# Performance work log

Measured on AMD Instinct MI355X. Metric: run time of the kernel, lower is better.

Reference implementation:

```python
import jax, jax.numpy as jnp
import numpy as np

L = 104          # atom feature / hidden dim (self.length)
NUM_CLASSES = 500
D, N, P = 256, 1024, 8  # DAGs, nodes per DAG (topo-ordered), max predecessors


def setup_inputs() -> dict:
    key = jax.random.key(0)
    ks = jax.random.split(key, 8)
    atom_features = jax.random.normal(ks[0], (D, N, L), dtype=jnp.float32)

    # Padded predecessor lists; pred_idx[d, n, p] < n guarantees topological order 0..N-1.
    rng = np.random.default_rng(0)
    base = np.floor(rng.random((D, N, P)) * np.maximum(np.arange(N), 1)[None, :, None]).astype(np.int32)
    keep = rng.random((D, N, P)) < 0.6
    keep[:, :, 0] = True                      # every non-root node has >=1 predecessor
    pred_idx = np.where(keep, base, -1)
    pred_idx[:, 0, :] = -1                    # node 0 is the root (no predecessors)
    pred_idx = jnp.asarray(pred_idx, dtype=jnp.int32)

    s1 = float(1.0 / np.sqrt(L))
    s2 = float(1.0 / np.sqrt(2 * L))
    W_single = jax.random.uniform(ks[1], (L, L), minval=-s1, maxval=s1)
    b_single = jax.random.uniform(ks[2], (L,), minval=-s1, maxval=s1)
    W_merge = jax.random.uniform(ks[3], (L, 2 * L), minval=-s2, maxval=s2)
    b_merge = jax.random.uniform(ks[4], (L,), minval=-s2, maxval=s2)
    attn_w = jax.random.uniform(ks[5], (L,))   # torch.rand(length)
    dag_w = jax.random.uniform(ks[6], (L,))
    W_final = jax.random.uniform(ks[7], (NUM_CLASSES, L), minval=-s1, maxval=s1)
    b_final = jnp.zeros((NUM_CLASSES,), jnp.float32)
    return {
        "atom_features": atom_features, "pred_idx": pred_idx,
        "W_single": W_single, "b_single": b_single,
        "W_merge": W_merge, "b_merge": b_merge,
        "attn_w": attn_w, "dag_w": dag_w,
        "W_final": W_final, "b_final": b_final,
    }


def _forward(atom_features, pred_idx, W_single, b_single, W_merge, b_merge,
             attn_w, dag_w, W_final, b_final):
    n_nodes = atom_features.shape[1]

    def per_dag(feats, preds):  # feats [N, L], preds [N, P]
        def step(outputs, n):
            feat = feats[n]                                   # [L]
            p = preds[n]                                      # [P]
            valid = p >= 0                                    # [P]
            po = outputs[jnp.clip(p, 0, n_nodes - 1)]         # [P, L] gathered predecessor outputs
            # softmax over the predecessor (stacking) dim, weighted by attention_weight
            logits = jnp.where(valid[:, None], attn_w * po, -1e30)
            agg = jnp.sum(jax.nn.softmax(logits, axis=0) * po * valid[:, None].astype(po.dtype), axis=0)  # [L]
            merged = jax.nn.relu(W_merge @ jnp.concatenate([agg, feat]) + b_merge)
            root = jax.nn.relu(W_single @ feat + b_single)
            out = jnp.where(jnp.any(valid), merged, root)     # [L]
            return outputs.at[n].set(out), None
        outputs, _ = jax.lax.scan(step, jnp.zeros_like(feats), jnp.arange(n_nodes))
        return outputs[-1]                                    # output of last (sink) node

    last = jax.vmap(per_dag)(atom_features, pred_idx)         # [D, L]
    w = jax.nn.softmax(dag_w * last, axis=0)                  # softmax over DAG dim
    pooled = jnp.sum(w * last, axis=0)                        # [L]
    return pooled @ W_final.T + b_final                       # [NUM_CLASSES]


def reference(atom_features, pred_idx, W_single, b_single, W_merge, b_merge,
              attn_w, dag_w, W_final, b_final):
    return _forward(atom_features, pred_idx, W_single, b_single, W_merge, b_merge,
                    attn_w, dag_w, W_final, b_final)
```

## Files before the change

kernel.cpp:

```cpp
#include <hip/hip_runtime.h>

#define DN  256
#define NN  1024
#define PP  8
#define LL  104
#define CLS 500
#define BT  512
#define TMAX 64
#define KP  232
#define NG  26
#define OLP 108
#define NEGBIG -3.0e38f

typedef __attribute__((ext_vector_type(8))) short short8;
typedef __attribute__((ext_vector_type(4))) short short4v;
typedef __attribute__((ext_vector_type(4))) float f32x4;

#define MFMA(a, b, c) __builtin_amdgcn_mfma_f32_16x16x32_bf16((a), (b), (c), 0, 0, 0)

#define BAR_RAW() do {                                              \
    __builtin_amdgcn_sched_barrier(0);                              \
    asm volatile("s_waitcnt lgkmcnt(0)" ::: "memory");              \
    __builtin_amdgcn_s_barrier();                                   \
    __builtin_amdgcn_sched_barrier(0);                              \
} while (0)

__device__ __forceinline__ void split_bf16(float x, unsigned short& h, unsigned short& l) {
    unsigned u = __float_as_uint(x);
    h = (unsigned short)(u >> 16);
    float hf = __uint_as_float(u & 0xFFFF0000u);
    l = (unsigned short)(__float_as_uint(x - hf) >> 16);
}

__device__ __forceinline__ void sm_store3(int ni, int lg, float4 aw4,
    const float4 pv[PP], float4 ft,
    unsigned short (*xh)[KP], unsigned short (*xl)[KP])
{
    float awv[4] = {aw4.x, aw4.y, aw4.z, aw4.w};
    float ftv[4] = {ft.x, ft.y, ft.z, ft.w};
    unsigned short oh[4], ol[4], fh[4], fl[4];
    #pragma unroll
    for (int f = 0; f < 4; ++f) {
        float den = 0.f, num = 0.f;
        #pragma unroll
        for (int q = 0; q < PP; ++q) {
            float pvq = ((const float*)&pv[q])[f];
            float e2 = exp2f(awv[f] * pvq);
            den += e2;
            num = fmaf(e2, pvq, num);
        }
        float agg = __fdividef(num, den);
        split_bf16(agg,    oh[f], ol[f]);
        split_bf16(ftv[f], fh[f], fl[f]);
    }
    *(short4v*)&xh[ni][lg*4] = (short4v){(short)oh[0],(short)oh[1],(short)oh[2],(short)oh[3]};
    *(short4v*)&xl[ni][lg*4] = (short4v){(short)ol[0],(short)ol[1],(short)ol[2],(short)ol[3]};
    *(short4v*)&xh[ni][LL + lg*4] = (short4v){(short)fh[0],(short)fh[1],(short)fh[2],(short)fh[3]};
    *(short4v*)&xl[ni][LL + lg*4] = (short4v){(short)fl[0],(short)fl[1],(short)fl[2],(short)fl[3]};
}

__global__ __launch_bounds__(BT, 2) void dag_level_kernel(
    const float* __restrict__ atom,
    const int*   __restrict__ pred,
    const float* __restrict__ W_single,
    const float* __restrict__ b_single,
    const float* __restrict__ W_merge,
    const float* __restrict__ b_merge,
    const float* __restrict__ attn_w,
    float* __restrict__ out_all,
    float* __restrict__ last_buf)
{
    __shared__ __align__(16) unsigned short x_hi[TMAX][KP];
    __shared__ __align__(16) unsigned short x_lo[TMAX][KP];
    __shared__ __align__(16) unsigned short ppos_lds[NN][PP];
    __shared__ __align__(16) float out_lds[2][TMAX][OLP];
    __shared__ int   lvl[NN];
    __shared__ int   cnt[NN];
    __shared__ unsigned short order[NN];
    __shared__ unsigned short pos_lds[NN];
    __shared__ __align__(16) float s_attn2[LL];
    __shared__ float s_bm[LL];
    __shared__ int   csum[64];
    __shared__ int   s_flag, s_maxlvl;

    const int d    = blockIdx.x;
    const int tid  = threadIdx.x;
    const int wid  = tid >> 6;
    const int lane = tid & 63;
    const int my_ni = tid / NG;
    const int my_lg = tid - my_ni * NG;

    const float* atom_d = atom + (size_t)d * NN * LL;
    const int*   pred_d = pred + (size_t)d * NN * PP;
    float*       out_d  = out_all + (size_t)d * NN * LL;

    short8 wh[7], wl[7];
    {
        const int r = min(wid, 6)*16 + (lane & 15);
        #pragma unroll
        for (int kt = 0; kt < 7; ++kt) {
            const int k0 = kt*32 + (lane >> 4)*8;
            short8 hh, lo8;
            #pragma unroll
            for (int j = 0; j < 8; ++j) {
                float v = (r < LL && (k0 + j) < 2*LL) ? W_merge[r*2*LL + k0 + j] : 0.f;
                unsigned short a, b;
                split_bf16(v, a, b);
                hh[j] = (short)a; lo8[j] = (short)b;
            }
            wh[kt] = hh; wl[kt] = lo8;
        }
    }

    for (int idx = tid; idx < TMAX * (KP - 2*LL); idx += BT) {
        int rr = idx / (KP - 2*LL), cc = 2*LL + (idx - rr*(KP - 2*LL));
        x_hi[rr][cc] = 0; x_lo[rr][cc] = 0;
    }
    if (tid < LL) {
        s_attn2[tid] = fmaxf(attn_w[tid] * 1.44269504f, 1e-30f);
        s_bm[tid] = b_merge[tid];
    }
    if (tid == 0) { s_flag = 0; s_maxlvl = 0; }
    lvl[tid] = 0; lvl[tid + BT] = 0;

    int mypA[PP], mypB[PP];
    {
        const int4* p4 = (const int4*)(pred_d + tid * PP);
        int4 a = p4[0], b = p4[1];
        mypA[0]=a.x; mypA[1]=a.y; mypA[2]=a.z; mypA[3]=a.w;
        mypA[4]=b.x; mypA[5]=b.y; mypA[6]=b.z; mypA[7]=b.w;
        const int4* q4 = (const int4*)(pred_d + (tid + BT) * PP);
        int4 c = q4[0], e = q4[1];
        mypB[0]=c.x; mypB[1]=c.y; mypB[2]=c.z; mypB[3]=c.w;
        mypB[4]=e.x; mypB[5]=e.y; mypB[6]=e.z; mypB[7]=e.w;
    }
    __syncthreads();

    for (int it = 1; it <= NN; ++it) {
        bool ch = false;
        #pragma unroll
        for (int rep = 0; rep < 2; ++rep) {
            int mxA = -1, mxB = -1;
            #pragma unroll
            for (int q = 0; q < PP; ++q) {
                if (mypA[q] >= 0) mxA = max(mxA, lvl[mypA[q]]);
                if (mypB[q] >= 0) mxB = max(mxB, lvl[mypB[q]]);
            }
            if (mxA + 1 != lvl[tid])      { lvl[tid]      = mxA + 1; ch = true; }
            if (mxB + 1 != lvl[tid + BT]) { lvl[tid + BT] = mxB + 1; ch = true; }
        }
        if (ch) s_flag = it;
        __syncthreads();
        int f = s_flag;
        __syncthreads();
        if (f != it) break;
    }
    atomicMax(&s_maxlvl, max(lvl[tid], lvl[tid + BT]));

    cnt[tid] = 0; cnt[tid + BT] = 0;
    __syncthreads();
    atomicAdd(&cnt[lvl[tid]], 1);
    atomicAdd(&cnt[lvl[tid + BT]], 1);
    __syncthreads();
    if (tid < 64) { int s = 0; for (int i = 0; i < 16; ++i) s += cnt[tid*16 + i]; csum[tid] = s; }
    __syncthreads();
    if (tid == 0) { int run = 0; for (int t = 0; t < 64; ++t) { int c = csum[t]; csum[t] = run; run += c; } }
    __syncthreads();
    if (tid < 64) {
        int run = csum[tid];
        for (int i = 0; i < 16; ++i) { int c = cnt[tid*16 + i]; cnt[tid*16 + i] = run; run += c; }
    }
    __syncthreads();
    {
        int pos = atomicAdd(&cnt[lvl[tid]], 1);
        order[pos] = (unsigned short)tid;        pos_lds[tid] = (unsigned short)pos;
        pos = atomicAdd(&cnt[lvl[tid + BT]], 1);
        order[pos] = (unsigned short)(tid + BT); pos_lds[tid + BT] = (unsigned short)pos;
    }
    __syncthreads();

    {
        unsigned short tA[PP], tB[PP];
        #pragma unroll
        for (int q = 0; q < PP; ++q) {
            tA[q] = (mypA[q] < 0) ? (unsigned short)0xFFFFu : pos_lds[mypA[q]];
            tB[q] = (mypB[q] < 0) ? (unsigned short)0xFFFFu : pos_lds[mypB[q]];
        }
        int pA = pos_lds[tid], pB = pos_lds[tid + BT];
        *(short4v*)&ppos_lds[pA][0] = (short4v){(short)tA[0],(short)tA[1],(short)tA[2],(short)tA[3]};
        *(short4v*)&ppos_lds[pA][4] = (short4v){(short)tA[4],(short)tA[5],(short)tA[6],(short)tA[7]};
        *(short4v*)&ppos_lds[pB][0] = (short4v){(short)tB[0],(short)tB[1],(short)tB[2],(short)tB[3]};
        *(short4v*)&ppos_lds[pB][4] = (short4v){(short)tB[4],(short)tB[5],(short)tB[6],(short)tB[7]};
    }
    __syncthreads();

    const float4 my_aw = *(const float4*)&s_attn2[my_lg * 4];

    {
        int nroots = cnt[0];
        for (int task = tid; task < nroots * LL; task += BT) {
            int ni = task / LL, r = task - ni * LL;
            int n = order[ni];
            float acc = b_single[r];
            const float* feat = atom_d + n * LL;
            const float* wr = W_single + r * LL;
            #pragma unroll 8
            for (int l = 0; l < LL; ++l) acc = fmaf(wr[l], feat[l], acc);
            float v = fmaxf(acc, 0.f);
            out_d[n * LL + r] = v;
            if (ni < TMAX) out_lds[1][ni][r] = v;
            if (n == NN - 1) last_buf[d * LL + r] = v;
        }
    }
    __syncthreads();

    const int maxlvl = s_maxlvl;

    float4  pf_po[PP];
    float4  pf_ft = {0.f,0.f,0.f,0.f};
    short8  pf_pps = {0,0,0,0,0,0,0,0};

#define PREFETCH(NT0, NTC, CT0, PT0, PBUF) do {                                \
        if (tid < (NTC) * NG) {                                                \
            int n_ = order[(NT0) + my_ni];                                     \
            pf_ft  = *(const float4*)&atom_d[n_ * LL + my_lg * 4];             \
            pf_pps = *(const short8*)&ppos_lds[(NT0) + my_ni][0];              \
            _Pragma("unroll")                                                  \
            for (int q_ = 0; q_ < PP; ++q_) {                                  \
                int pp_ = (unsigned short)pf_pps[q_];                          \
                if (pp_ >= (CT0)) {                                            \
                    pf_po[q_] = (float4){NEGBIG, NEGBIG, NEGBIG, NEGBIG};      \
                } else if (pp_ >= (PT0)) {                                     \
                    pf_po[q_] = *(const float4*)&out_lds[PBUF][pp_ - (PT0)][my_lg * 4]; \
                } else {                                                       \
                    pf_po[q_] = *(const float4*)&out_d[(int)order[pp_] * LL + my_lg * 4]; \
                }                                                              \
            }                                                                  \
        }                                                                      \
    } while (0)

    int pt0 = 0, ptc = cnt[0];
    int wbuf = 0;

    if (maxlvl >= 1) {
        int s1 = cnt[0];
        PREFETCH(s1, min(TMAX, cnt[1] - s1), s1, 0, 1);
    }

    for (int L = 1; L <= maxlvl; ++L) {
        const int s = cnt[L - 1], e = cnt[L];
        for (int t0 = s; t0 < e; t0 += TMAX) {
            const int tc = min(TMAX, e - t0);
            const int ntask = tc * NG;
            const int pcopy = ptc * NG;
            const int rbuf = wbuf ^ 1;

            for (int ct = tid; ct < pcopy; ct += BT) {
                int ci = ct / NG, lg2 = ct - ci * NG;
                *(float4*)&out_d[(int)order[pt0 + ci] * LL + lg2 * 4] =
                    *(const float4*)&out_lds[rbuf][ci][lg2 * 4];
            }
            if (tid < ntask) {
                float4 pv[PP];
                #pragma unroll
                for (int q = 0; q < PP; ++q) {
                    int pp = (unsigned short)pf_pps[q];
                    bool fresh = (pp >= pt0) && (pp < t0);
                    int slot = fresh ? (pp - pt0) : 0;
                    float4 lv = *(const float4*)&out_lds[rbuf][slot][my_lg * 4];
                    pv[q] = fresh ? lv : pf_po[q];
                }
                sm_store3(my_ni, my_lg, my_aw, pv, pf_ft, x_hi, x_lo);
            }
            for (int task = tid + BT; task < ntask; task += BT) {
                int ni = task / NG, lg = task - ni * NG;
                short8 pps = *(const short8*)&ppos_lds[t0 + ni][0];
                float4 pv[PP];
                #pragma unroll
                for (int q = 0; q < PP; ++q) {
                    int pp = (unsigned short)pps[q];
                    if (pp >= t0) {
                        pv[q] = (float4){NEGBIG, NEGBIG, NEGBIG, NEGBIG};
                    } else if (pp >= pt0) {
                        pv[q] = *(const float4*)&out_lds[rbuf][pp - pt0][lg * 4];
                    } else {
                        pv[q] = *(const float4*)&out_d[(int)order[pp] * LL + lg * 4];
                    }
                }
                int n = order[t0 + ni];
                float4 ft = *(const float4*)&atom_d[n * LL + lg * 4];
                float4 aw4 = *(const float4*)&s_attn2[lg * 4];
                sm_store3(ni, lg, aw4, pv, ft, x_hi, x_lo);
            }
            __syncthreads();

            {
                int nt0 = 0, ntc = 0;
                if (t0 + TMAX < e)        { nt0 = t0 + TMAX; ntc = min(TMAX, e - nt0); }
                else if (L + 1 <= maxlvl) { nt0 = e;         ntc = min(TMAX, cnt[L + 1] - e); }
                PREFETCH(nt0, ntc, t0, pt0, rbuf);
            }

            if (wid < 7) {
                const int mts = (tc + 15) >> 4;
                const int kg = (lane >> 4) * 8;
                const int r0 = wid*16 + (lane & 15);
                for (int mt = 0; mt < mts; ++mt) {
                    const int row_a = mt*16 + (lane & 15);
                    f32x4 a0 = {0.f,0.f,0.f,0.f}, b0 = {0.f,0.f,0.f,0.f}, c0 = {0.f,0.f,0.f,0.f};
                    #pragma unroll
                    for (int kt = 0; kt < 7; ++kt) {
                        const int k0 = kt*32 + kg;
                        short8 ah = *(const short8*)&x_hi[row_a][k0];
                        short8 al = *(const short8*)&x_lo[row_a][k0];
                        a0 = MFMA(ah, wh[kt], a0);
                        b0 = MFMA(ah, wl[kt], b0);
                        c0 = MFMA(al, wh[kt], c0);
                    }
                    f32x4 acc = a0 + b0 + c0;
                    if (r0 < LL) {
                        #pragma unroll
                        for (int j = 0; j < 4; ++j) {
                            int ni = mt*16 + (lane >> 4)*4 + j;
                            if (ni < tc) {
                                float v = fmaxf(acc[j] + s_bm[r0], 0.f);
                                out_lds[wbuf][ni][r0] = v;
                                int n = order[t0 + ni];
                                if (n == NN - 1) last_buf[d*LL + r0] = v;
                            }
                        }
                    }
                }
            }
            BAR_RAW();
            pt0 = t0; ptc = tc; wbuf ^= 1;
        }
    }
#undef PREFETCH
}

__global__ __launch_bounds__(256) void final_pool_kernel(
    const float* __restrict__ last_buf,
    const float* __restrict__ dag_w,
    const float* __restrict__ W_final,
    const float* __restrict__ b_final,
    float* __restrict__ out)
{
    __shared__ float s_pooled[LL];
    const int tid = threadIdx.x;

    if (tid < LL) {
        float dw = dag_w[tid];
        float m = -1e30f;
        #pragma unroll 8
        for (int dd = 0; dd < DN; ++dd)
            m = fmaxf(m, dw * last_buf[dd * LL + tid]);
        float den = 0.f, num = 0.f;
        #pragma unroll 8
        for (int dd = 0; dd < DN; ++dd) {
            float v = last_buf[dd * LL + tid];
            float e = __expf(dw * v - m);
            den += e;
            num = fmaf(e, v, num);
        }
        s_pooled[tid] = num / den;
    }
    __syncthreads();

    for (int c = tid; c < CLS; c += 256) {
        float acc = b_final[c];
        const float* wr = W_final + c * LL;
        #pragma unroll 8
        for (int l = 0; l < LL; ++l) acc = fmaf(wr[l], s_pooled[l], acc);
        out[c] = acc;
    }
}

extern "C" void kernel_launch(void* const* d_in, const int* in_sizes, int n_in,
                              void* d_out, int out_size, void* d_ws, size_t ws_size,
                              hipStream_t stream) {
    const float* atom     = (const float*)d_in[0];
    const int*   pred     = (const int*)  d_in[1];
    const float* W_single = (const float*)d_in[2];
    const float* b_single = (const float*)d_in[3];
    const float* W_merge  = (const float*)d_in[4];
    const float* b_merge  = (const float*)d_in[5];
    const float* attn_w   = (const float*)d_in[6];
    const float* dag_w    = (const float*)d_in[7];
    const float* W_final  = (const float*)d_in[8];
    const float* b_final  = (const float*)d_in[9];
    float* out = (float*)d_out;

    float* out_all  = (float*)d_ws;
    float* last_buf = out_all + (size_t)DN * NN * LL;

    dag_level_kernel<<<DN, BT, 0, stream>>>(atom, pred, W_single, b_single,
                                            W_merge, b_merge, attn_w,
                                            out_all, last_buf);
    final_pool_kernel<<<1, 256, 0, stream>>>(last_buf, dag_w, W_final, b_final, out);
}
```

Measured before the change: 378.8 us.

## Accumulate prefetched softmax partials incrementally instead of holding raw predecessor vectors

The prefetch stage now folds the exp2 numerator and denominator of already-available predecessors into running float4 partial sums, and pre-splits features into bf16 hi/lo halves. It no longer keeps eight raw float4 predecessor rows in registers. The global-memory loads are issued before the MFMA section and consumed after it, so their latency is hidden behind the matrix work. The intent is to cut register pressure and shorten the serial aggregation after the barrier. In exchange, the code is more complex and masks invalid entries with NEGBIG exponent inputs instead of using branches.

Measured after the change: 400.9 us. 5.8% more time.

```diff
diff --git a/kernel.cpp b/kernel.cpp
--- a/kernel.cpp
+++ b/kernel.cpp
@@ -32,31 +32,37 @@
     l = (unsigned short)(__float_as_uint(x - hf) >> 16);
 }
 
-__device__ __forceinline__ void sm_store3(int ni, int lg, float4 aw4,
-    const float4 pv[PP], float4 ft,
-    unsigned short (*xh)[KP], unsigned short (*xl)[KP])
+__device__ __forceinline__ void split4(float4 v, short4v& h4, short4v& l4) {
+    unsigned short h0,h1,h2,h3,l0,l1,l2,l3;
+    split_bf16(v.x,h0,l0); split_bf16(v.y,h1,l1);
+    split_bf16(v.z,h2,l2); split_bf16(v.w,h3,l3);
+    h4 = (short4v){(short)h0,(short)h1,(short)h2,(short)h3};
+    l4 = (short4v){(short)l0,(short)l1,(short)l2,(short)l3};
+}
+
+__device__ __forceinline__ void acc4(float4& num, float4& den, float4 aw, float4 v, bool on) {
+    float e0 = __builtin_amdgcn_exp2f(on ? aw.x*v.x : NEGBIG);
+    float e1 = __builtin_amdgcn_exp2f(on ? aw.y*v.y : NEGBIG);
+    float e2 = __builtin_amdgcn_exp2f(on ? aw.z*v.z : NEGBIG);
+    float e3 = __builtin_amdgcn_exp2f(on ? aw.w*v.w : NEGBIG);
+    den.x += e0; den.y += e1; den.z += e2; den.w += e3;
+    num.x = fmaf(e0, v.x, num.x);
+    num.y = fmaf(e1, v.y, num.y);
+    num.z = fmaf(e2, v.z, num.z);
+    num.w = fmaf(e3, v.w, num.w);
+}
+
+__device__ __forceinline__ void store_x(int ni, int lg, float4 num, float4 den,
+    short4v fth, short4v ftl, unsigned short (*xh)[KP], unsigned short (*xl)[KP])
 {
-    float awv[4] = {aw4.x, aw4.y, aw4.z, aw4.w};
-    float ftv[4] = {ft.x, ft.y, ft.z, ft.w};
-    unsigned short oh[4], ol[4], fh[4], fl[4];
-    #pragma unroll
-    for (int f = 0; f < 4; ++f) {
-        float den = 0.f, num = 0.f;
-        #pragma unroll
-        for (int q = 0; q < PP; ++q) {
-            float pvq = ((const float*)&pv[q])[f];
-            float e2 = exp2f(awv[f] * pvq);
-            den += e2;
-            num = fmaf(e2, pvq, num);
-        }
-        float agg = __fdividef(num, den);
-        split_bf16(agg,    oh[f], ol[f]);
-        split_bf16(ftv[f], fh[f], fl[f]);
-    }
-    *(short4v*)&xh[ni][lg*4] = (short4v){(short)oh[0],(short)oh[1],(short)oh[2],(short)oh[3]};
-    *(short4v*)&xl[ni][lg*4] = (short4v){(short)ol[0],(short)ol[1],(short)ol[2],(short)ol[3]};
-    *(short4v*)&xh[ni][LL + lg*4] = (short4v){(short)fh[0],(short)fh[1],(short)fh[2],(short)fh[3]};
-    *(short4v*)&xl[ni][LL + lg*4] = (short4v){(short)fl[0],(short)fl[1],(short)fl[2],(short)fl[3]};
+    float4 agg = { __fdividef(num.x, den.x), __fdividef(num.y, den.y),
+                   __fdividef(num.z, den.z), __fdividef(num.w, den.w) };
+    short4v ah, al;
+    split4(agg, ah, al);
+    *(short4v*)&xh[ni][lg*4] = ah;
+    *(short4v*)&xl[ni][lg*4] = al;
+    *(short4v*)&xh[ni][LL + lg*4] = fth;
+    *(short4v*)&xl[ni][LL + lg*4] = ftl;
 }
 
 __global__ __launch_bounds__(BT, 2) void dag_level_kernel(
@@ -216,35 +222,22 @@
 
     const int maxlvl = s_maxlvl;
 
-    float4  pf_po[PP];
-    float4  pf_ft = {0.f,0.f,0.f,0.f};
+    float4  pf_num = {0,0,0,0}, pf_den = {0,0,0,0};
+    short4v pf_fth = {0,0,0,0}, pf_ftl = {0,0,0,0};
     short8  pf_pps = {0,0,0,0,0,0,0,0};
-
-#define PREFETCH(NT0, NTC, CT0, PT0, PBUF) do {                                \
-        if (tid < (NTC) * NG) {                                                \
-            int n_ = order[(NT0) + my_ni];                                     \
-            pf_ft  = *(const float4*)&atom_d[n_ * LL + my_lg * 4];             \
-            pf_pps = *(const short8*)&ppos_lds[(NT0) + my_ni][0];              \
-            _Pragma("unroll")                                                  \
-            for (int q_ = 0; q_ < PP; ++q_) {                                  \
-                int pp_ = (unsigned short)pf_pps[q_];                          \
-                if (pp_ >= (CT0)) {                                            \
-                    pf_po[q_] = (float4){NEGBIG, NEGBIG, NEGBIG, NEGBIG};      \
-                } else if (pp_ >= (PT0)) {                                     \
-                    pf_po[q_] = *(const float4*)&out_lds[PBUF][pp_ - (PT0)][my_lg * 4]; \
-                } else {                                                       \
-                    pf_po[q_] = *(const float4*)&out_d[(int)order[pp_] * LL + my_lg * 4]; \
-                }                                                              \
-            }                                                                  \
-        }                                                                      \
-    } while (0)
 
     int pt0 = 0, ptc = cnt[0];
     int wbuf = 0;
 
     if (maxlvl >= 1) {
         int s1 = cnt[0];
-        PREFETCH(s1, min(TMAX, cnt[1] - s1), s1, 0, 1);
+        int ntc0 = min(TMAX, cnt[1] - s1);
+        if (tid < ntc0 * NG) {
+            int n_ = order[s1 + my_ni];
+            float4 ft = *(const float4*)&atom_d[n_ * LL + my_lg * 4];
+            split4(ft, pf_fth, pf_ftl);
+            pf_pps = *(const short8*)&ppos_lds[s1 + my_ni][0];
+        }
     }
 
     for (int L = 1; L <= maxlvl; ++L) {
@@ -261,44 +254,79 @@
                     *(const float4*)&out_lds[rbuf][ci][lg2 * 4];
             }
             if (tid < ntask) {
-                float4 pv[PP];
+                float4 num = pf_num, den = pf_den;
                 #pragma unroll
                 for (int q = 0; q < PP; ++q) {
                     int pp = (unsigned short)pf_pps[q];
                     bool fresh = (pp >= pt0) && (pp < t0);
                     int slot = fresh ? (pp - pt0) : 0;
                     float4 lv = *(const float4*)&out_lds[rbuf][slot][my_lg * 4];
-                    pv[q] = fresh ? lv : pf_po[q];
-                }
-                sm_store3(my_ni, my_lg, my_aw, pv, pf_ft, x_hi, x_lo);
+                    acc4(num, den, my_aw, lv, fresh);
+                }
+                store_x(my_ni, my_lg, num, den, pf_fth, pf_ftl, x_hi, x_lo);
             }
             for (int task = tid + BT; task < ntask; task += BT) {
                 int ni = task / NG, lg = task - ni * NG;
                 short8 pps = *(const short8*)&ppos_lds[t0 + ni][0];
-                float4 pv[PP];
+                float4 aw4 = *(const float4*)&s_attn2[lg * 4];
+                float4 gv2[PP];
                 #pragma unroll
                 for (int q = 0; q < PP; ++q) {
                     int pp = (unsigned short)pps[q];
-                    if (pp >= t0) {
-                        pv[q] = (float4){NEGBIG, NEGBIG, NEGBIG, NEGBIG};
-                    } else if (pp >= pt0) {
-                        pv[q] = *(const float4*)&out_lds[rbuf][pp - pt0][lg * 4];
-                    } else {
-                        pv[q] = *(const float4*)&out_d[(int)order[pp] * LL + lg * 4];
-                    }
+                    bool old = pp < pt0;
+                    int row = old ? (int)order[pp] : 0;
+                    gv2[q] = *(const float4*)&out_d[row * LL + lg * 4];
+                }
+                float4 num = {0,0,0,0}, den = {0,0,0,0};
+                #pragma unroll
+                for (int q = 0; q < PP; ++q) {
+                    int pp = (unsigned short)pps[q];
+                    bool on   = pp < t0;
+                    bool prev = pp >= pt0;
+                    int slot = (prev && on) ? (pp - pt0) : 0;
+                    float4 lv = *(const float4*)&out_lds[rbuf][slot][lg * 4];
+                    float4 v;
+                    v.x = prev ? lv.x : gv2[q].x; v.y = prev ? lv.y : gv2[q].y;
+                    v.z = prev ? lv.z : gv2[q].z; v.w = prev ? lv.w : gv2[q].w;
+                    acc4(num, den, aw4, v, on);
                 }
                 int n = order[t0 + ni];
                 float4 ft = *(const float4*)&atom_d[n * LL + lg * 4];
-                float4 aw4 = *(const float4*)&s_attn2[lg * 4];
-                sm_store3(ni, lg, aw4, pv, ft, x_hi, x_lo);
+                short4v fth, ftl;
+                split4(ft, fth, ftl);
+                store_x(ni, lg, num, den, fth, ftl, x_hi, x_lo);
             }
             __syncthreads();
 
-            {
-                int nt0 = 0, ntc = 0;
-                if (t0 + TMAX < e)        { nt0 = t0 + TMAX; ntc = min(TMAX, e - nt0); }
-                else if (L + 1 <= maxlvl) { nt0 = e;         ntc = min(TMAX, cnt[L + 1] - e); }
-                PREFETCH(nt0, ntc, t0, pt0, rbuf);
+            int nt0 = 0, ntc = 0;
+            if (t0 + TMAX < e)        { nt0 = t0 + TMAX; ntc = min(TMAX, e - nt0); }
+            else if (L + 1 <= maxlvl) { nt0 = e;         ntc = min(TMAX, cnt[L + 1] - e); }
+            const bool pf_act = tid < ntc * NG;
+
+            float4 gv[PP];
+            float4 ft4 = {0.f, 0.f, 0.f, 0.f};
+            if (pf_act) {
+                int n_ = order[nt0 + my_ni];
+                ft4 = *(const float4*)&atom_d[n_ * LL + my_lg * 4];
+                pf_pps = *(const short8*)&ppos_lds[nt0 + my_ni][0];
+                #pragma unroll
+                for (int q = 0; q < PP; ++q) {
+                    int pp = (unsigned short)pf_pps[q];
+                    bool old = pp < pt0;
+                    int row = old ? (int)order[pp] : 0;
+                    gv[q] = *(const float4*)&out_d[row * LL + my_lg * 4];
+                }
+            }
+            pf_num = (float4){0,0,0,0}; pf_den = (float4){0,0,0,0};
+            if (pf_act) {
+                #pragma unroll
+                for (int q = 0; q < PP; ++q) {
+                    int pp = (unsigned short)pf_pps[q];
+                    bool prev = (pp >= pt0) && (pp < t0);
+                    int slot = prev ? (pp - pt0) : 0;
+                    float4 lv = *(const float4*)&out_lds[rbuf][slot][my_lg * 4];
+                    acc4(pf_num, pf_den, my_aw, lv, prev);
+                }
             }
 
             if (wid < 7) {
@@ -332,11 +360,21 @@
                     }
                 }
             }
+
+            if (pf_act) {
+                #pragma unroll
+                for (int q = 0; q < PP; ++q) {
+                    int pp = (unsigned short)pf_pps[q];
+                    bool old = pp < pt0;
+                    acc4(pf_num, pf_den, my_aw, gv[q], old);
+                }
+                split4(ft4, pf_fth, pf_ftl);
+            }
+
             BAR_RAW();
             pt0 = t0; ptc = tc; wbuf ^= 1;
         }
     }
-#undef PREFETCH
 }
 
 __global__ __launch_bounds__(256) void final_pool_kernel(
```

## Split softmax aggregation into float2 tasks with two prefetched sets per thread

Applied to the files above, without the earlier changes.

Each node's feature group now covers 2 floats instead of 4, so the aggregation work splits into twice as many tasks, and each thread prefetches two task sets (A and B) during the MFMA phase instead of one. The feature bf16 split moves into the prefetch, the exp2 uses the hardware builtin, and the fallback loop becomes branch-free with masked exp. The aim is to spread the serial softmax/gather phase over all 512 threads for tiles of up to 64 nodes and to hide more latency behind the matmul. In exchange it uses more registers for the doubled prefetch state, which could hurt occupancy under launch_bounds(512,2).

New measurement: 387.0 us. +2.2%, slower.

```diff
diff --git a/kernel.cpp b/kernel.cpp
--- a/kernel.cpp
+++ b/kernel.cpp
@@ -8,7 +8,8 @@
 #define BT  512
 #define TMAX 64
 #define KP  232
-#define NG  26
+#define NG2 52
+#define NGC 26
 #define OLP 108
 #define NEGBIG -3.0e38f
 
@@ -32,31 +33,32 @@
     l = (unsigned short)(__float_as_uint(x - hf) >> 16);
 }
 
-__device__ __forceinline__ void sm_store3(int ni, int lg, float4 aw4,
-    const float4 pv[PP], float4 ft,
-    unsigned short (*xh)[KP], unsigned short (*xl)[KP])
+__device__ __forceinline__ void acc2(float2& num, float2& den, float2 aw, float2 v) {
+    float e0 = __builtin_amdgcn_exp2f(aw.x * v.x);
+    float e1 = __builtin_amdgcn_exp2f(aw.y * v.y);
+    den.x += e0; den.y += e1;
+    num.x = fmaf(e0, v.x, num.x);
+    num.y = fmaf(e1, v.y, num.y);
+}
+__device__ __forceinline__ void acc2m(float2& num, float2& den, float2 aw, float2 v, bool on) {
+    float e0 = __builtin_amdgcn_exp2f(on ? aw.x * v.x : NEGBIG);
+    float e1 = __builtin_amdgcn_exp2f(on ? aw.y * v.y : NEGBIG);
+    den.x += e0; den.y += e1;
+    num.x = fmaf(e0, v.x, num.x);
+    num.y = fmaf(e1, v.y, num.y);
+}
+
+__device__ __forceinline__ void store_x2(int ni, int lg, float2 num, float2 den,
+    unsigned fth, unsigned ftl, unsigned short (*xh)[KP], unsigned short (*xl)[KP])
 {
-    float awv[4] = {aw4.x, aw4.y, aw4.z, aw4.w};
-    float ftv[4] = {ft.x, ft.y, ft.z, ft.w};
-    unsigned short oh[4], ol[4], fh[4], fl[4];
-    #pragma unroll
-    for (int f = 0; f < 4; ++f) {
-        float den = 0.f, num = 0.f;
-        #pragma unroll
-        for (int q = 0; q < PP; ++q) {
-            float pvq = ((const float*)&pv[q])[f];
-            float e2 = exp2f(awv[f] * pvq);
-            den += e2;
-            num = fmaf(e2, pvq, num);
-        }
-        float agg = __fdividef(num, den);
-        split_bf16(agg,    oh[f], ol[f]);
-        split_bf16(ftv[f], fh[f], fl[f]);
-    }
-    *(short4v*)&xh[ni][lg*4] = (short4v){(short)oh[0],(short)oh[1],(short)oh[2],(short)oh[3]};
-    *(short4v*)&xl[ni][lg*4] = (short4v){(short)ol[0],(short)ol[1],(short)ol[2],(short)ol[3]};
-    *(short4v*)&xh[ni][LL + lg*4] = (short4v){(short)fh[0],(short)fh[1],(short)fh[2],(short)fh[3]};
-    *(short4v*)&xl[ni][LL + lg*4] = (short4v){(short)fl[0],(short)fl[1],(short)fl[2],(short)fl[3]};
+    float ax = __fdividef(num.x, den.x);
+    float ay = __fdividef(num.y, den.y);
+    unsigned short h0, l0, h1, l1;
+    split_bf16(ax, h0, l0); split_bf16(ay, h1, l1);
+    *(unsigned*)&xh[ni][lg*2] = (unsigned)h0 | ((unsigned)h1 << 16);
+    *(unsigned*)&xl[ni][lg*2] = (unsigned)l0 | ((unsigned)l1 << 16);
+    *(unsigned*)&xh[ni][LL + lg*2] = fth;
+    *(unsigned*)&xl[ni][LL + lg*2] = ftl;
 }
 
 __global__ __launch_bounds__(BT, 2) void dag_level_kernel(
@@ -87,8 +89,8 @@
     const int tid  = threadIdx.x;
     const int wid  = tid >> 6;
     const int lane = tid & 63;
-    const int my_ni = tid / NG;
-    const int my_lg = tid - my_ni * NG;
+    const int niA = tid / NG2,        lgA = tid - niA * NG2;
+    const int niB = (tid+BT) / NG2,   lgB = (tid+BT) - niB * NG2;
 
     const float* atom_d = atom + (size_t)d * NN * LL;
     const int*   pred_d = pred + (size_t)d * NN * PP;
@@ -194,7 +196,8 @@
     }
     __syncthreads();
 
-    const float4 my_aw = *(const float4*)&s_attn2[my_lg * 4];
+    const float2 awA = *(const float2*)&s_attn2[lgA * 2];
+    const float2 awB = *(const float2*)&s_attn2[lgB * 2];
 
     {
         int nroots = cnt[0];
@@ -216,24 +219,28 @@
 
     const int maxlvl = s_maxlvl;
 
-    float4  pf_po[PP];
-    float4  pf_ft = {0.f,0.f,0.f,0.f};
-    short8  pf_pps = {0,0,0,0,0,0,0,0};
-
-#define PREFETCH(NT0, NTC, CT0, PT0, PBUF) do {                                \
-        if (tid < (NTC) * NG) {                                                \
-            int n_ = order[(NT0) + my_ni];                                     \
-            pf_ft  = *(const float4*)&atom_d[n_ * LL + my_lg * 4];             \
-            pf_pps = *(const short8*)&ppos_lds[(NT0) + my_ni][0];              \
+    float2  pfA_po[PP], pfB_po[PP];
+    unsigned pfA_fth = 0, pfA_ftl = 0, pfB_fth = 0, pfB_ftl = 0;
+    short8  pf_ppsA = {0,0,0,0,0,0,0,0}, pf_ppsB = {0,0,0,0,0,0,0,0};
+
+#define PREFETCH_SET(PPS, PO, FTH, FTL, TASK, NI, LG, NT0, NTC, CT0, PT0, PBUF) do { \
+        if ((TASK) < (NTC) * NG2) {                                            \
+            int n_ = order[(NT0) + (NI)];                                      \
+            float2 ft_ = *(const float2*)&atom_d[n_ * LL + (LG) * 2];          \
+            unsigned short a0_, a1_, b0_, b1_;                                 \
+            split_bf16(ft_.x, a0_, b0_); split_bf16(ft_.y, a1_, b1_);          \
+            FTH = (unsigned)a0_ | ((unsigned)a1_ << 16);                       \
+            FTL = (unsigned)b0_ | ((unsigned)b1_ << 16);                       \
+            PPS = *(const short8*)&ppos_lds[(NT0) + (NI)][0];                  \
             _Pragma("unroll")                                                  \
             for (int q_ = 0; q_ < PP; ++q_) {                                  \
-                int pp_ = (unsigned short)pf_pps[q_];                          \
+                int pp_ = (unsigned short)PPS[q_];                             \
                 if (pp_ >= (CT0)) {                                            \
-                    pf_po[q_] = (float4){NEGBIG, NEGBIG, NEGBIG, NEGBIG};      \
+                    PO[q_] = (float2){NEGBIG, NEGBIG};                         \
                 } else if (pp_ >= (PT0)) {                                     \
-                    pf_po[q_] = *(const float4*)&out_lds[PBUF][pp_ - (PT0)][my_lg * 4]; \
+                    PO[q_] = *(const float2*)&out_lds[PBUF][pp_ - (PT0)][(LG) * 2]; \
                 } else {                                                       \
-                    pf_po[q_] = *(const float4*)&out_d[(int)order[pp_] * LL + my_lg * 4]; \
+                    PO[q_] = *(const float2*)&out_d[(int)order[pp_] * LL + (LG) * 2]; \
                 }                                                              \
             }                                                                  \
         }                                                                      \
@@ -244,53 +251,83 @@
 
     if (maxlvl >= 1) {
         int s1 = cnt[0];
-        PREFETCH(s1, min(TMAX, cnt[1] - s1), s1, 0, 1);
+        int ntc0 = min(TMAX, cnt[1] - s1);
+        PREFETCH_SET(pf_ppsA, pfA_po, pfA_fth, pfA_ftl, tid,      niA, lgA, s1, ntc0, s1, 0, 1);
+        PREFETCH_SET(pf_ppsB, pfB_po, pfB_fth, pfB_ftl, tid + BT, niB, lgB, s1, ntc0, s1, 0, 1);
     }
 
     for (int L = 1; L <= maxlvl; ++L) {
         const int s = cnt[L - 1], e = cnt[L];
         for (int t0 = s; t0 < e; t0 += TMAX) {
             const int tc = min(TMAX, e - t0);
-            const int ntask = tc * NG;
-            const int pcopy = ptc * NG;
+            const int ntask = tc * NG2;
+            const int pcopy = ptc * NGC;
             const int rbuf = wbuf ^ 1;
 
             for (int ct = tid; ct < pcopy; ct += BT) {
-                int ci = ct / NG, lg2 = ct - ci * NG;
-                *(float4*)&out_d[(int)order[pt0 + ci] * LL + lg2 * 4] =
-                    *(const float4*)&out_lds[rbuf][ci][lg2 * 4];
+                int ci = ct / NGC, lgc = ct - ci * NGC;
+                *(float4*)&out_d[(int)order[pt0 + ci] * LL + lgc * 4] =
+                    *(const float4*)&out_lds[rbuf][ci][lgc * 4];
             }
             if (tid < ntask) {
-                float4 pv[PP];
+                float2 num = {0.f, 0.f}, den = {0.f, 0.f};
                 #pragma unroll
                 for (int q = 0; q < PP; ++q) {
-                    int pp = (unsigned short)pf_pps[q];
+                    int pp = (unsigned short)pf_ppsA[q];
                     bool fresh = (pp >= pt0) && (pp < t0);
                     int slot = fresh ? (pp - pt0) : 0;
-                    float4 lv = *(const float4*)&out_lds[rbuf][slot][my_lg * 4];
-                    pv[q] = fresh ? lv : pf_po[q];
+                    float2 lv = *(const float2*)&out_lds[rbuf][slot][lgA * 2];
+                    float2 v; v.x = fresh ? lv.x : pfA_po[q].x;
+                              v.y = fresh ? lv.y : pfA_po[q].y;
+                    acc2(num, den, awA, v);
                 }
-                sm_store3(my_ni, my_lg, my_aw, pv, pf_ft, x_hi, x_lo);
-            }
-            for (int task = tid + BT; task < ntask; task += BT) {
-                int ni = task / NG, lg = task - ni * NG;
+                store_x2(niA, lgA, num, den, pfA_fth, pfA_ftl, x_hi, x_lo);
+            }
+            if (tid + BT < ntask) {
+                float2 num = {0.f, 0.f}, den = {0.f, 0.f};
+                #pragma unroll
+                for (int q = 0; q < PP; ++q) {
+                    int pp = (unsigned short)pf_ppsB[q];
+                    bool fresh = (pp >= pt0) && (pp < t0);
+                    int slot = fresh ? (pp - pt0) : 0;
+                    float2 lv = *(const float2*)&out_lds[rbuf][slot][lgB * 2];
+                    float2 v; v.x = fresh ? lv.x : pfB_po[q].x;
+                              v.y = fresh ? lv.y : pfB_po[q].y;
+                    acc2(num, den, awB, v);
+                }
+                store_x2(niB, lgB, num, den, pfB_fth, pfB_ftl, x_hi, x_lo);
+            }
+            for (int task = tid + 2*BT; task < ntask; task += BT) {
+                int ni = task / NG2, lg = task - ni * NG2;
                 short8 pps = *(const short8*)&ppos_lds[t0 + ni][0];
-                float4 pv[PP];
+                float2 aw = *(const float2*)&s_attn2[lg * 2];
+                float2 gv[PP];
                 #pragma unroll
                 for (int q = 0; q < PP; ++q) {
                     int pp = (unsigned short)pps[q];
-                    if (pp >= t0) {
-                        pv[q] = (float4){NEGBIG, NEGBIG, NEGBIG, NEGBIG};
-                    } else if (pp >= pt0) {
-                        pv[q] = *(const float4*)&out_lds[rbuf][pp - pt0][lg * 4];
-                    } else {
-                        pv[q] = *(const float4*)&out_d[(int)order[pp] * LL + lg * 4];
-                    }
+                    bool old = pp < pt0;
+                    int row = old ? (int)order[pp] : 0;
+                    gv[q] = *(const float2*)&out_d[row * LL + lg * 2];
+                }
+                float2 num = {0.f, 0.f}, den = {0.f, 0.f};
+                #pragma unroll
+                for (int q = 0; q < PP; ++q) {
+                    int pp = (unsigned short)pps[q];
+                    bool on   = pp < t0;
+                    bool prev = pp >= pt0;
+                    int slot = (prev && on) ? (pp - pt0) : 0;
+                    float2 lv = *(const float2*)&out_lds[rbuf][slot][lg * 2];
+                    float2 v; v.x = prev ? lv.x : gv[q].x;
+                              v.y = prev ? lv.y : gv[q].y;
+                    acc2m(num, den, aw, v, on);
                 }
                 int n = order[t0 + ni];
-                float4 ft = *(const float4*)&atom_d[n * LL + lg * 4];
-                float4 aw4 = *(const float4*)&s_attn2[lg * 4];
-                sm_store3(ni, lg, aw4, pv, ft, x_hi, x_lo);
+                float2 ft = *(const float2*)&atom_d[n * LL + lg * 2];
+                unsigned short a0, a1, b0, b1;
+                split_bf16(ft.x, a0, b0); split_bf16(ft.y, a1, b1);
+                unsigned fth = (unsigned)a0 | ((unsigned)a1 << 16);
+                unsigned ftl = (unsigned)b0 | ((unsigned)b1 << 16);
+                store_x2(ni, lg, num, den, fth, ftl, x_hi, x_lo);
             }
             __syncthreads();
 
@@ -298,7 +335,8 @@
                 int nt0 = 0, ntc = 0;
                 if (t0 + TMAX < e)        { nt0 = t0 + TMAX; ntc = min(TMAX, e - nt0); }
                 else if (L + 1 <= maxlvl) { nt0 = e;         ntc = min(TMAX, cnt[L + 1] - e); }
-                PREFETCH(nt0, ntc, t0, pt0, rbuf);
+                PREFETCH_SET(pf_ppsA, pfA_po, pfA_fth, pfA_ftl, tid,      niA, lgA, nt0, ntc, t0, pt0, rbuf);
+                PREFETCH_SET(pf_ppsB, pfB_po, pfB_fth, pfB_ftl, tid + BT, niB, lgB, nt0, ntc, t0, pt0, rbuf);
             }
 
             if (wid < 7) {
@@ -336,7 +374,7 @@
             pt0 = t0; ptc = tc; wbuf ^= 1;
         }
     }
-#undef PREFETCH
+#undef PREFETCH_SET
 }
 
 __global__ __launch_bounds__(256) void final_pool_kernel(
```
